# Optimization experiments

Measured on AMD Instinct MI355X. Metric: run time of the kernel, lower is better.

The kernel has to match this reference:

```python
import jax, jax.numpy as jnp
import numpy as np

N_NODES = 50000
N_EDGES = 800000
NFEAT, NHID, IN_HEAD, NCLASS, OUT_HEAD = 256, 16, 8, 47, 1
NEG_SLOPE = 0.2


def setup_inputs() -> dict:
    key = jax.random.key(0)
    ks = jax.random.split(key, 10)
    x = jax.random.normal(ks[0], (N_NODES, NFEAT), dtype=jnp.float32)
    edge_index = jax.random.randint(ks[1], (2, N_EDGES), 0, N_NODES, dtype=jnp.int64)
    W1 = jax.random.normal(ks[2], (NFEAT, IN_HEAD * NHID), dtype=jnp.float32) * 0.06
    a1_src = jax.random.normal(ks[3], (IN_HEAD, NHID), dtype=jnp.float32) * 0.25
    a1_dst = jax.random.normal(ks[4], (IN_HEAD, NHID), dtype=jnp.float32) * 0.25
    b1 = jax.random.normal(ks[5], (IN_HEAD * NHID,), dtype=jnp.float32) * 0.02
    W2 = jax.random.normal(ks[6], (IN_HEAD * NHID, NCLASS), dtype=jnp.float32) * 0.09
    a2_src = jax.random.normal(ks[7], (OUT_HEAD, NCLASS), dtype=jnp.float32) * 0.15
    a2_dst = jax.random.normal(ks[8], (OUT_HEAD, NCLASS), dtype=jnp.float32) * 0.15
    b2 = jax.random.normal(ks[9], (NCLASS,), dtype=jnp.float32) * 0.02
    return {"x": x, "edge_index": edge_index, "W1": W1, "a1_src": a1_src,
            "a1_dst": a1_dst, "b1": b1, "W2": W2, "a2_src": a2_src,
            "a2_dst": a2_dst, "b2": b2}


def _gat_layer(x, W, a_src, a_dst, b, src, dst, n_nodes, concat):
    # x: [N, F_in]; W: [F_in, H*C]; a_*: [H, C]
    H, C = a_src.shape
    h = (x @ W).reshape(n_nodes, H, C)                        # [N, H, C]
    # per-node partial attention logits, then gather per edge
    s_src = jnp.einsum('nhc,hc->nh', h, a_src)                # [N, H]
    s_dst = jnp.einsum('nhc,hc->nh', h, a_dst)                # [N, H]
    e = jax.nn.leaky_relu(s_src[src] + s_dst[dst], NEG_SLOPE) # [E, H]
    # segment softmax over destination node
    m = jax.ops.segment_max(e, dst, num_segments=n_nodes)     # [N, H]
    ex = jnp.exp(e - m[dst])
    denom = jax.ops.segment_sum(ex, dst, num_segments=n_nodes)
    alpha = ex / (denom[dst] + 1e-16)                         # [E, H]
    # weighted message aggregation (scatter-add)
    msg = alpha[:, :, None] * h[src]                          # [E, H, C]
    out = jax.ops.segment_sum(msg, dst, num_segments=n_nodes) # [N, H, C]
    out = out.reshape(n_nodes, H * C) if concat else out.mean(axis=1)
    return out + b


def reference(x, edge_index, W1, a1_src, a1_dst, b1, W2, a2_src, a2_dst, b2):
    n = x.shape[0]
    # PyG GATConv default: add self-loops
    loops = jnp.arange(n, dtype=edge_index.dtype)
    src = jnp.concatenate([edge_index[0], loops])
    dst = jnp.concatenate([edge_index[1], loops])
    # eval mode: dropout is identity
    h = _gat_layer(x, W1, a1_src, a1_dst, b1, src, dst, n, concat=True)
    h = jax.nn.elu(h)
    out = _gat_layer(h, W2, a2_src, a2_dst, b2, src, dst, n, concat=False)
    return jax.nn.log_softmax(out, axis=1)
```

## Files before the change

### kernel.cpp

```cpp
#include <hip/hip_runtime.h>
#include <hip/hip_fp16.h>

#define N_NODES 50000
#define N_EDGES 800000
#define E2 (N_EDGES + N_NODES)

#define BSHIFT 6
#define BMASK 63
#define NBUCK 782
#define EPB 4096
#define NBLKC 208

typedef _Float16 h8v __attribute__((ext_vector_type(8)));
typedef float f4v __attribute__((ext_vector_type(4)));


__global__ __launch_bounds__(256) void k_hist(const int* __restrict__ ei,
                                              int* __restrict__ gh) {
    __shared__ int h[NBUCK];
    int tid = threadIdx.x;
    for (int b = tid; b < NBUCK; b += 256) h[b] = 0;
    __syncthreads();
    int base = blockIdx.x * EPB;
    for (int i = tid; i < EPB; i += 256) {
        int e = base + i;
        if (e < E2) {
            int dst = (e < N_EDGES) ? ei[N_EDGES + e] : (e - N_EDGES);
            atomicAdd(&h[dst >> BSHIFT], 1);
        }
    }
    __syncthreads();
    for (int b = tid; b < NBUCK; b += 256) gh[blockIdx.x * NBUCK + b] = h[b];
}

__global__ __launch_bounds__(256) void k_colscan(int* __restrict__ gh,
                                                 int* __restrict__ tot) {
    int wave = threadIdx.x >> 6, lane = threadIdx.x & 63;
    int b = blockIdx.x * 4 + wave;
    if (b >= NBUCK) return;
    int carry = 0;
    for (int c = 0; c < NBLKC; c += 64) {
        int k = c + lane;
        int v = (k < NBLKC) ? gh[k * NBUCK + b] : 0;
        int x = v;
        #pragma unroll
        for (int o = 1; o < 64; o <<= 1) { int y = __shfl_up(x, o); if (lane >= o) x += y; }
        if (k < NBLKC) gh[k * NBUCK + b] = carry + x - v;
        carry += __shfl(x, 63);
    }
    if (lane == 0) tot[b] = carry;
}

__global__ __launch_bounds__(1024) void k_btot(const int* __restrict__ tot,
        int* __restrict__ boff, const float* __restrict__ W2, float* __restrict__ W2p) {
    int t = threadIdx.x;
    for (int i = t; i < 128 * 48; i += 1024) {
        int k = i / 48, c = i - k * 48;
        W2p[i] = (c < 47) ? W2[k * 47 + c] : 0.f;
    }
    int v = (t < NBUCK) ? tot[t] : 0;
    __shared__ int ws[16];
    int lane = t & 63, w = t >> 6;
    int x = v;
    #pragma unroll
    for (int o = 1; o < 64; o <<= 1) { int y = __shfl_up(x, o); if (lane >= o) x += y; }
    if (lane == 63) ws[w] = x;
    __syncthreads();
    if (t == 0) {
        #pragma unroll
        for (int j = 1; j < 16; ++j) ws[j] += ws[j - 1];
    }
    __syncthreads();
    int add = (w == 0) ? 0 : ws[w - 1];
    int excl = add + x - v;
    if (t < NBUCK) boff[t] = excl;
    if (t == NBUCK - 1) boff[NBUCK] = excl + v;
}

__global__ __launch_bounds__(256) void k_place(const int* __restrict__ ei,
        const int* __restrict__ gh, const int* __restrict__ boff,
        unsigned int* __restrict__ brec) {
    __shared__ int sbase[NBUCK];
    __shared__ int cnt[NBUCK];
    int tid = threadIdx.x;
    for (int b = tid; b < NBUCK; b += 256) {
        sbase[b] = boff[b] + gh[blockIdx.x * NBUCK + b];
        cnt[b] = 0;
    }
    __syncthreads();
    int base = blockIdx.x * EPB;
    for (int i = tid; i < EPB; i += 256) {
        int e = base + i;
        if (e < E2) {
            int src, dst;
            if (e < N_EDGES) { src = ei[e]; dst = ei[N_EDGES + e]; }
            else             { src = dst = e - N_EDGES; }
            int b = dst >> BSHIFT;
            int r = atomicAdd(&cnt[b], 1);
            brec[sbase[b] + r] = ((unsigned int)(dst & BMASK) << 16) | (unsigned int)src;
        }
    }
}

__global__ __launch_bounds__(256) void k_finalize(const unsigned int* __restrict__ brec,
        const int* __restrict__ boff, unsigned short* __restrict__ csr_src,
        int* __restrict__ offs) {
    int B = blockIdx.x;
    int tid = threadIdx.x;
    int base = boff[B];
    int total = boff[B + 1] - base;
    __shared__ int hist[64], cur[64];
    __shared__ unsigned short stage[2048];
    if (tid < 64) hist[tid] = 0;
    __syncthreads();
    const unsigned int* bp = brec + base;
    for (int i = tid; i < total; i += 256) atomicAdd(&hist[bp[i] >> 16], 1);
    __syncthreads();
    if (tid < 64) {
        int v = hist[tid];
        int x = v;
        #pragma unroll
        for (int o = 1; o < 64; o <<= 1) { int y = __shfl_up(x, o); if (tid >= o) x += y; }
        int excl = x - v;
        cur[tid] = excl;
        int n = B * 64 + tid;
        if (n < N_NODES) offs[n] = base + excl;
    }
    if (B == NBUCK - 1 && tid == 0) offs[N_NODES] = boff[NBUCK];
    __syncthreads();
    if (total <= 2048) {
        for (int i = tid; i < total; i += 256) {
            unsigned int r = bp[i];
            int p = atomicAdd(&cur[r >> 16], 1);
            stage[p] = (unsigned short)(r & 0xFFFFu);
        }
        __syncthreads();
        for (int i = tid; i < total; i += 256) csr_src[base + i] = stage[i];
    } else {
        for (int i = tid; i < total; i += 256) {
            unsigned int r = bp[i];
            int p = atomicAdd(&cur[r >> 16], 1);
            csr_src[base + p] = (unsigned short)(r & 0xFFFFu);
        }
    }
}


__global__ void k_prepw1(const float* __restrict__ W1, _Float16* __restrict__ W1T) {
    int i = blockIdx.x * 256 + threadIdx.x;
    if (i >= 128 * 256) return;
    int c = i >> 8, k = i & 255;
    W1T[i] = (_Float16)W1[k * 128 + c];
}


__global__ __launch_bounds__(128) void k_gemm1(const float* __restrict__ x,
        const _Float16* __restrict__ W1T, _Float16* __restrict__ h1h) {
    int lane = threadIdx.x & 63;
    int wv = threadIdx.x >> 6;
    int rowbase = blockIdx.x * 64 + wv * 32;
    int r0 = lane & 15;
    int kg = lane >> 4;
    f4v acc[2][8];
    #pragma unroll
    for (int i = 0; i < 2; ++i)
        #pragma unroll
        for (int j = 0; j < 8; ++j) acc[i][j] = (f4v)0.f;

    #pragma unroll 1
    for (int kt = 0; kt < 256; kt += 32) {
        h8v a[2];
        #pragma unroll
        for (int rf = 0; rf < 2; ++rf) {
            int row = rowbase + rf * 16 + r0;
            if (row >= N_NODES) row = N_NODES - 1;
            const float* ap = x + (size_t)row * 256 + kt + kg * 8;
            float4 lo = *(const float4*)ap;
            float4 hi = *(const float4*)(ap + 4);
            h8v t;
            t[0] = (_Float16)lo.x; t[1] = (_Float16)lo.y;
            t[2] = (_Float16)lo.z; t[3] = (_Float16)lo.w;
            t[4] = (_Float16)hi.x; t[5] = (_Float16)hi.y;
            t[6] = (_Float16)hi.z; t[7] = (_Float16)hi.w;
            a[rf] = t;
        }
        #pragma unroll
        for (int cf = 0; cf < 8; ++cf) {
            h8v b = *(const h8v*)(W1T + (size_t)(cf * 16 + r0) * 256 + kt + kg * 8);
            acc[0][cf] = __builtin_amdgcn_mfma_f32_16x16x32_f16(a[0], b, acc[0][cf], 0, 0, 0);
            acc[1][cf] = __builtin_amdgcn_mfma_f32_16x16x32_f16(a[1], b, acc[1][cf], 0, 0, 0);
        }
    }
    #pragma unroll
    for (int rf = 0; rf < 2; ++rf) {
        #pragma unroll
        for (int r = 0; r < 4; ++r) {
            int row = rowbase + rf * 16 + kg * 4 + r;
            if (row < N_NODES) {
                _Float16* orow = h1h + (size_t)row * 128 + r0;
                #pragma unroll
                for (int cf = 0; cf < 8; ++cf)
                    orow[cf * 16] = (_Float16)acc[rf][cf][r];
            }
        }
    }
}


__global__ void k_logits1(const __half* __restrict__ h1h,
                          const float* __restrict__ a1s, const float* __restrict__ a1d,
                          float* __restrict__ s1s, float* __restrict__ s1d) {
    int idx = blockIdx.x * blockDim.x + threadIdx.x;
    if (idx >= N_NODES * 8) return;
    int n = idx >> 3, h = idx & 7;
    const __half2* hp2 = (const __half2*)(h1h + (size_t)n * 128 + h * 16);
    float ss = 0.f, sd = 0.f;
    #pragma unroll
    for (int c2 = 0; c2 < 8; ++c2) {
        float2 v = __half22float2(hp2[c2]);
        ss += v.x * a1s[h * 16 + 2 * c2] + v.y * a1s[h * 16 + 2 * c2 + 1];
        sd += v.x * a1d[h * 16 + 2 * c2] + v.y * a1d[h * 16 + 2 * c2 + 1];
    }
    s1s[idx] = ss;
    s1d[idx] = sd;
}


__global__ __launch_bounds__(256) void k_agg1(const __half* __restrict__ h1h,
        const float* __restrict__ s1s, const float* __restrict__ s1d,
        const int* __restrict__ offs, const unsigned short* __restrict__ csr_src,
        const float* __restrict__ b1, float* __restrict__ h2o) {
    int wave = threadIdx.x >> 6;
    int lane = threadIdx.x & 63;
    int n = blockIdx.x * 4 + wave;
    int beg = offs[n];
    int deg = offs[n + 1] - beg;

    int h = lane & 7;
    int slot = lane >> 3;
    int grp = lane >> 4;
    int cidx = lane & 15;
    int hc = cidx >> 1;
    float sdh = s1d[n * 8 + h];

    float dsum = 0.f;
    float acc[8] = {0.f, 0.f, 0.f, 0.f, 0.f, 0.f, 0.f, 0.f};
    for (int chunk = 0; chunk < deg; chunk += 8) {
        int i = chunk + slot;
        int esrc = csr_src[beg + ((i < deg) ? i : (deg - 1))];
        float aN = 0.f;
        if (i < deg) {
            float e = s1s[esrc * 8 + h] + sdh;
            e = (e > 0.f) ? e : 0.2f * e;
            aN = __expf(e);
            dsum += aN;
        }
        int   src0 = __shfl(esrc, (grp) * 8);
        float a0   = __shfl(aN, (grp) * 8 + hc);
        int   src1 = __shfl(esrc, (4 + grp) * 8);
        float a1   = __shfl(aN, (4 + grp) * 8 + hc);
        h8v v0 = *(const h8v*)(h1h + (size_t)src0 * 128 + cidx * 8);
        h8v v1 = *(const h8v*)(h1h + (size_t)src1 * 128 + cidx * 8);
        #pragma unroll
        for (int j = 0; j < 8; ++j) acc[j] += a0 * (float)v0[j];
        #pragma unroll
        for (int j = 0; j < 8; ++j) acc[j] += a1 * (float)v1[j];
    }
    dsum += __shfl_xor(dsum, 8);
    dsum += __shfl_xor(dsum, 16);
    dsum += __shfl_xor(dsum, 32);
    float rd = 1.f / __shfl(dsum, hc);
    #pragma unroll
    for (int j = 0; j < 8; ++j) {
        acc[j] += __shfl_xor(acc[j], 16);
        acc[j] += __shfl_xor(acc[j], 32);
    }
    int c0 = cidx * 8 + grp * 2;
    float va = acc[grp * 2] * rd + b1[c0];
    va = (va > 0.f) ? va : (__expf(va) - 1.f);
    float vb = acc[grp * 2 + 1] * rd + b1[c0 + 1];
    vb = (vb > 0.f) ? vb : (__expf(vb) - 1.f);
    *(float2*)(h2o + (size_t)n * 128 + c0) = make_float2(va, vb);
}


__global__ __launch_bounds__(256) void k_gemm2(const float* __restrict__ h2,
        const float* __restrict__ W2p,
        const float* __restrict__ a2s, const float* __restrict__ a2d,
        __half* __restrict__ g2h, float* __restrict__ s2s, float* __restrict__ s2d) {
    int n = blockIdx.x * 256 + threadIdx.x;
    bool valid = (n < N_NODES);
    int nn = valid ? n : (N_NODES - 1);
    const float* hrow = h2 + (size_t)nn * 128;
    float4 acc[12];
    #pragma unroll
    for (int j = 0; j < 12; ++j) acc[j] = make_float4(0.f, 0.f, 0.f, 0.f);
    #pragma unroll 1
    for (int k = 0; k < 128; k += 4) {
        float4 hv = *(const float4*)(hrow + k);
        float hk[4] = {hv.x, hv.y, hv.z, hv.w};
        #pragma unroll
        for (int kk = 0; kk < 4; ++kk) {
            const float* wrow = W2p + (size_t)(k + kk) * 48;
            #pragma unroll
            for (int j = 0; j < 12; ++j) {
                float4 wv = *(const float4*)(wrow + j * 4);
                acc[j].x += hk[kk] * wv.x;
                acc[j].y += hk[kk] * wv.y;
                acc[j].z += hk[kk] * wv.z;
                acc[j].w += hk[kk] * wv.w;
            }
        }
    }
    float vs = 0.f, vd = 0.f;
    #pragma unroll
    for (int j = 0; j < 12; ++j) {
        int c = j * 4;
        vs += acc[j].x * a2s[c + 0]; vd += acc[j].x * a2d[c + 0];
        vs += acc[j].y * a2s[c + 1]; vd += acc[j].y * a2d[c + 1];
        vs += acc[j].z * a2s[c + 2]; vd += acc[j].z * a2d[c + 2];
        if (j < 11) { vs += acc[j].w * a2s[c + 3]; vd += acc[j].w * a2d[c + 3]; }
    }
    if (valid) {
        __half2* orow = (__half2*)(g2h + (size_t)n * 48);
        #pragma unroll
        for (int j = 0; j < 12; ++j) {
            orow[j * 2 + 0] = __floats2half2_rn(acc[j].x, acc[j].y);
            orow[j * 2 + 1] = __floats2half2_rn(acc[j].z, acc[j].w);
        }
        s2s[n] = vs;
        s2d[n] = vd;
    }
}


__global__ __launch_bounds__(256) void k_agg2(const __half* __restrict__ g2h,
        const float* __restrict__ s2s, const float* __restrict__ s2d,
        const int* __restrict__ offs, const unsigned short* __restrict__ csr_src,
        const float* __restrict__ b2, float* __restrict__ outp) {
    int wave = threadIdx.x >> 6, lane = threadIdx.x & 63;
    int n = blockIdx.x * 4 + wave;
    int beg = offs[n];
    int deg = offs[n + 1] - beg;
    float sdn = s2d[n];
    int c = (lane < 47) ? lane : 47;

    float dsum = 0.f;
    float acc = 0.f;
    for (int chunk = 0; chunk < deg; chunk += 64) {
        int i = chunk + lane;
        int esrc = csr_src[beg + ((i < deg) ? i : (deg - 1))];
        float aN = 0.f;
        if (i < deg) {
            float e = s2s[esrc] + sdn;
            e = (e > 0.f) ? e : 0.2f * e;
            aN = __expf(e);
            dsum += aN;
        }
        int lim = deg - chunk; if (lim > 64) lim = 64;
        for (int g = 0; g < lim; g += 8) {
            int   srcs[8];
            float as[8];
            #pragma unroll
            for (int s = 0; s < 8; ++s) {
                srcs[s] = __shfl(esrc, g + s);
                as[s]   = __shfl(aN, g + s);
            }
            __half v[8];
            #pragma unroll
            for (int s = 0; s < 8; ++s) v[s] = g2h[(size_t)srcs[s] * 48 + c];
            #pragma unroll
            for (int s = 0; s < 8; ++s) acc += as[s] * __half2float(v[s]);
        }
    }
    #pragma unroll
    for (int o = 32; o; o >>= 1) dsum += __shfl_xor(dsum, o);
    acc *= 1.f / dsum;

    float l = (lane < 47) ? acc + b2[lane] : -1e30f;
    float rm = l;
    #pragma unroll
    for (int o = 32; o; o >>= 1) rm = fmaxf(rm, __shfl_xor(rm, o));
    float p = (lane < 47) ? __expf(l - rm) : 0.f;
    float ps = p;
    #pragma unroll
    for (int o = 32; o; o >>= 1) ps += __shfl_xor(ps, o);
    float lse = rm + __logf(ps);
    if (lane < 47) outp[(size_t)n * 47 + lane] = l - lse;
}


extern "C" void kernel_launch(void* const* d_in, const int* in_sizes, int n_in,
                              void* d_out, int out_size, void* d_ws, size_t ws_size,
                              hipStream_t stream) {
    const float* x   = (const float*)d_in[0];
    const int*   ei  = (const int*)d_in[1];
    const float* W1  = (const float*)d_in[2];
    const float* a1s = (const float*)d_in[3];
    const float* a1d = (const float*)d_in[4];
    const float* b1  = (const float*)d_in[5];
    const float* W2  = (const float*)d_in[6];
    const float* a2s = (const float*)d_in[7];
    const float* a2d = (const float*)d_in[8];
    const float* b2  = (const float*)d_in[9];
    float* outp = (float*)d_out;

    char* ws = (char*)d_ws;
    size_t off = 0;
    auto alloc = [&](size_t bytes) -> void* {
        void* p = ws + off;
        off += (bytes + 255) & ~(size_t)255;
        return p;
    };
    int* gh      = (int*)alloc((size_t)NBLKC * NBUCK * 4);
    int* tot     = (int*)alloc((size_t)NBUCK * 4);
    int* boff    = (int*)alloc((size_t)(NBUCK + 1) * 4);
    unsigned int* brec = (unsigned int*)alloc((size_t)E2 * 4);
    unsigned short* csr_src = (unsigned short*)alloc((size_t)E2 * 2);
    int* offs    = (int*)alloc((size_t)(N_NODES + 1) * 4);
    __half* h1h  = (__half*)alloc((size_t)N_NODES * 128 * 2);
    float* s1s   = (float*)alloc((size_t)N_NODES * 8 * 4);
    float* s1d   = (float*)alloc((size_t)N_NODES * 8 * 4);
    float* h2    = (float*)alloc((size_t)N_NODES * 128 * 4);
    __half* g2h  = (__half*)alloc((size_t)N_NODES * 48 * 2);
    float* s2s   = (float*)alloc((size_t)N_NODES * 4);
    float* s2d   = (float*)alloc((size_t)N_NODES * 4);
    float* W2p   = (float*)alloc((size_t)128 * 48 * 4);
    _Float16* W1T = (_Float16*)alloc((size_t)128 * 256 * 2);

    (void)in_sizes; (void)n_in; (void)out_size; (void)ws_size;

    k_prepw1<<<128, 256, 0, stream>>>(W1, W1T);
    k_hist<<<NBLKC, 256, 0, stream>>>(ei, gh);
    k_colscan<<<(NBUCK + 3) / 4, 256, 0, stream>>>(gh, tot);
    k_btot<<<1, 1024, 0, stream>>>(tot, boff, W2, W2p);
    k_place<<<NBLKC, 256, 0, stream>>>(ei, gh, boff, brec);
    k_finalize<<<NBUCK, 256, 0, stream>>>(brec, boff, csr_src, offs);

    k_gemm1<<<(N_NODES + 63) / 64, 128, 0, stream>>>(x, W1T, (_Float16*)h1h);
    k_logits1<<<(N_NODES * 8 + 255) / 256, 256, 0, stream>>>(h1h, a1s, a1d, s1s, s1d);
    k_agg1<<<N_NODES / 4, 256, 0, stream>>>(h1h, s1s, s1d, offs, csr_src, b1, h2);

    k_gemm2<<<(N_NODES + 255) / 256, 256, 0, stream>>>(h2, W2p, a2s, a2d, g2h, s2s, s2d);
    k_agg2<<<N_NODES / 4, 256, 0, stream>>>(g2h, s2s, s2d, offs, csr_src, b2, outp);
}
```

Baseline: 179.9 us.

## Store layer-1 output in fp16, unroll agg1 gather, fold W1 prep into hist

The ELU output of the first aggregation is now stored as fp16 instead of fp32, and the second GEMM reads it as half2. This halves that intermediate's write and read traffic at some cost in precision. The agg1 edge loop now handles 16 edges per iteration with four independent row gathers, giving more memory-level parallelism. The W1 transpose kernel is merged into an extra block of the histogram kernel, which saves one launch.

```diff
diff --git a/kernel.cpp b/kernel.cpp
--- a/kernel.cpp
+++ b/kernel.cpp
@@ -16,7 +16,14 @@
 
 
 __global__ __launch_bounds__(256) void k_hist(const int* __restrict__ ei,
-                                              int* __restrict__ gh) {
+        int* __restrict__ gh, const float* __restrict__ W1, _Float16* __restrict__ W1T) {
+    if (blockIdx.x == NBLKC) {
+        for (int i = threadIdx.x; i < 128 * 256; i += 256) {
+            int c = i >> 8, k = i & 255;
+            W1T[i] = (_Float16)W1[k * 128 + c];
+        }
+        return;
+    }
     __shared__ int h[NBUCK];
     int tid = threadIdx.x;
     for (int b = tid; b < NBUCK; b += 256) h[b] = 0;
@@ -143,14 +150,6 @@
             csr_src[base + p] = (unsigned short)(r & 0xFFFFu);
         }
     }
-}
-
-
-__global__ void k_prepw1(const float* __restrict__ W1, _Float16* __restrict__ W1T) {
-    int i = blockIdx.x * 256 + threadIdx.x;
-    if (i >= 128 * 256) return;
-    int c = i >> 8, k = i & 255;
-    W1T[i] = (_Float16)W1[k * 128 + c];
 }
 
 
@@ -229,7 +228,7 @@
 __global__ __launch_bounds__(256) void k_agg1(const __half* __restrict__ h1h,
         const float* __restrict__ s1s, const float* __restrict__ s1d,
         const int* __restrict__ offs, const unsigned short* __restrict__ csr_src,
-        const float* __restrict__ b1, float* __restrict__ h2o) {
+        const float* __restrict__ b1, __half* __restrict__ h2o) {
     int wave = threadIdx.x >> 6;
     int lane = threadIdx.x & 63;
     int n = blockIdx.x * 4 + wave;
@@ -245,26 +244,40 @@
 
     float dsum = 0.f;
     float acc[8] = {0.f, 0.f, 0.f, 0.f, 0.f, 0.f, 0.f, 0.f};
-    for (int chunk = 0; chunk < deg; chunk += 8) {
-        int i = chunk + slot;
-        int esrc = csr_src[beg + ((i < deg) ? i : (deg - 1))];
-        float aN = 0.f;
-        if (i < deg) {
-            float e = s1s[esrc * 8 + h] + sdh;
+    for (int chunk = 0; chunk < deg; chunk += 16) {
+        int i0 = chunk + slot;
+        int i1 = chunk + 8 + slot;
+        int e0 = csr_src[beg + ((i0 < deg) ? i0 : (deg - 1))];
+        int e1 = csr_src[beg + ((i1 < deg) ? i1 : (deg - 1))];
+        float a0 = 0.f, a1 = 0.f;
+        if (i0 < deg) {
+            float e = s1s[e0 * 8 + h] + sdh;
             e = (e > 0.f) ? e : 0.2f * e;
-            aN = __expf(e);
-            dsum += aN;
-        }
-        int   src0 = __shfl(esrc, (grp) * 8);
-        float a0   = __shfl(aN, (grp) * 8 + hc);
-        int   src1 = __shfl(esrc, (4 + grp) * 8);
-        float a1   = __shfl(aN, (4 + grp) * 8 + hc);
-        h8v v0 = *(const h8v*)(h1h + (size_t)src0 * 128 + cidx * 8);
-        h8v v1 = *(const h8v*)(h1h + (size_t)src1 * 128 + cidx * 8);
-        #pragma unroll
-        for (int j = 0; j < 8; ++j) acc[j] += a0 * (float)v0[j];
-        #pragma unroll
-        for (int j = 0; j < 8; ++j) acc[j] += a1 * (float)v1[j];
+            a0 = __expf(e);
+            dsum += a0;
+        }
+        if (i1 < deg) {
+            float e = s1s[e1 * 8 + h] + sdh;
+            e = (e > 0.f) ? e : 0.2f * e;
+            a1 = __expf(e);
+            dsum += a1;
+        }
+        int   s0 = __shfl(e0, grp * 8);       float w0 = __shfl(a0, grp * 8 + hc);
+        int   s1 = __shfl(e0, (4 + grp) * 8); float w1 = __shfl(a0, (4 + grp) * 8 + hc);
+        int   s2 = __shfl(e1, grp * 8);       float w2 = __shfl(a1, grp * 8 + hc);
+        int   s3 = __shfl(e1, (4 + grp) * 8); float w3 = __shfl(a1, (4 + grp) * 8 + hc);
+        h8v v0 = *(const h8v*)(h1h + (size_t)s0 * 128 + cidx * 8);
+        h8v v1 = *(const h8v*)(h1h + (size_t)s1 * 128 + cidx * 8);
+        h8v v2 = *(const h8v*)(h1h + (size_t)s2 * 128 + cidx * 8);
+        h8v v3 = *(const h8v*)(h1h + (size_t)s3 * 128 + cidx * 8);
+        #pragma unroll
+        for (int j = 0; j < 8; ++j) acc[j] += w0 * (float)v0[j];
+        #pragma unroll
+        for (int j = 0; j < 8; ++j) acc[j] += w1 * (float)v1[j];
+        #pragma unroll
+        for (int j = 0; j < 8; ++j) acc[j] += w2 * (float)v2[j];
+        #pragma unroll
+        for (int j = 0; j < 8; ++j) acc[j] += w3 * (float)v3[j];
     }
     dsum += __shfl_xor(dsum, 8);
     dsum += __shfl_xor(dsum, 16);
@@ -280,25 +293,26 @@
     va = (va > 0.f) ? va : (__expf(va) - 1.f);
     float vb = acc[grp * 2 + 1] * rd + b1[c0 + 1];
     vb = (vb > 0.f) ? vb : (__expf(vb) - 1.f);
-    *(float2*)(h2o + (size_t)n * 128 + c0) = make_float2(va, vb);
-}
-
-
-__global__ __launch_bounds__(256) void k_gemm2(const float* __restrict__ h2,
+    *(__half2*)(h2o + (size_t)n * 128 + c0) = __floats2half2_rn(va, vb);
+}
+
+
+__global__ __launch_bounds__(256) void k_gemm2(const __half* __restrict__ h2,
         const float* __restrict__ W2p,
         const float* __restrict__ a2s, const float* __restrict__ a2d,
         __half* __restrict__ g2h, float* __restrict__ s2s, float* __restrict__ s2d) {
     int n = blockIdx.x * 256 + threadIdx.x;
     bool valid = (n < N_NODES);
     int nn = valid ? n : (N_NODES - 1);
-    const float* hrow = h2 + (size_t)nn * 128;
+    const __half2* hrow = (const __half2*)(h2 + (size_t)nn * 128);
     float4 acc[12];
     #pragma unroll
     for (int j = 0; j < 12; ++j) acc[j] = make_float4(0.f, 0.f, 0.f, 0.f);
     #pragma unroll 1
     for (int k = 0; k < 128; k += 4) {
-        float4 hv = *(const float4*)(hrow + k);
-        float hk[4] = {hv.x, hv.y, hv.z, hv.w};
+        float2 h01 = __half22float2(hrow[k / 2]);
+        float2 h23 = __half22float2(hrow[k / 2 + 1]);
+        float hk[4] = {h01.x, h01.y, h23.x, h23.y};
         #pragma unroll
         for (int kk = 0; kk < 4; ++kk) {
             const float* wrow = W2p + (size_t)(k + kk) * 48;
@@ -421,7 +435,7 @@
     __half* h1h  = (__half*)alloc((size_t)N_NODES * 128 * 2);
     float* s1s   = (float*)alloc((size_t)N_NODES * 8 * 4);
     float* s1d   = (float*)alloc((size_t)N_NODES * 8 * 4);
-    float* h2    = (float*)alloc((size_t)N_NODES * 128 * 4);
+    __half* h2h  = (__half*)alloc((size_t)N_NODES * 128 * 2);
     __half* g2h  = (__half*)alloc((size_t)N_NODES * 48 * 2);
     float* s2s   = (float*)alloc((size_t)N_NODES * 4);
     float* s2d   = (float*)alloc((size_t)N_NODES * 4);
@@ -430,8 +444,7 @@
 
     (void)in_sizes; (void)n_in; (void)out_size; (void)ws_size;
 
-    k_prepw1<<<128, 256, 0, stream>>>(W1, W1T);
-    k_hist<<<NBLKC, 256, 0, stream>>>(ei, gh);
+    k_hist<<<NBLKC + 1, 256, 0, stream>>>(ei, gh, W1, W1T);
     k_colscan<<<(NBUCK + 3) / 4, 256, 0, stream>>>(gh, tot);
     k_btot<<<1, 1024, 0, stream>>>(tot, boff, W2, W2p);
     k_place<<<NBLKC, 256, 0, stream>>>(ei, gh, boff, brec);
@@ -439,8 +452,8 @@
 
     k_gemm1<<<(N_NODES + 63) / 64, 128, 0, stream>>>(x, W1T, (_Float16*)h1h);
     k_logits1<<<(N_NODES * 8 + 255) / 256, 256, 0, stream>>>(h1h, a1s, a1d, s1s, s1d);
-    k_agg1<<<N_NODES / 4, 256, 0, stream>>>(h1h, s1s, s1d, offs, csr_src, b1, h2);
-
-    k_gemm2<<<(N_NODES + 255) / 256, 256, 0, stream>>>(h2, W2p, a2s, a2d, g2h, s2s, s2d);
+    k_agg1<<<N_NODES / 4, 256, 0, stream>>>(h1h, s1s, s1d, offs, csr_src, b1, h2h);
+
+    k_gemm2<<<(N_NODES + 255) / 256, 256, 0, stream>>>(h2h, W2p, a2s, a2d, g2h, s2s, s2d);
     k_agg2<<<N_NODES / 4, 256, 0, stream>>>(g2h, s2s, s2d, offs, csr_src, b2, outp);
 }
```

After: 178.4 us, median of 2. Within noise of the previous version (-0.9%).
